# Optimization experiments

Hardware: AMD Instinct MI355X
Metric: run time of the kernel (lower is better)

The kernel has to match this reference:

```python
import jax, jax.numpy as jnp
import numpy as np

B, C, L, H, W = 4, 128, 8, 64, 64

def setup_inputs() -> dict:
    key = jax.random.key(0)
    ks = jax.random.split(key, 9)
    s = 0.05
    return {
        'feats': jax.random.normal(ks[0], (B, C, L, H, W), jnp.float32),
        'proj_w': jax.random.normal(ks[1], (C, C, L), jnp.float32) * s,  # Conv3d kernel (band,1,1) collapsing l
        'proj_b': jax.random.normal(ks[2], (C,), jnp.float32) * s,
        'w1': jax.random.normal(ks[3], (C, C), jnp.float32) * s,
        'b1': jax.random.normal(ks[4], (C,), jnp.float32) * s,
        'w2': jax.random.normal(ks[5], (C, C), jnp.float32) * s,
        'b2': jax.random.normal(ks[6], (C,), jnp.float32) * s,
        'w3': jax.random.normal(ks[7], (C, C), jnp.float32) * s,
        'b3': jax.random.normal(ks[8], (C,), jnp.float32) * s,
        'alpha': jnp.zeros((1,), jnp.float32),
    }

def reference(feats, proj_w, proj_b, w1, b1, w2, b2, w3, b3, alpha):
    b, c, l, h, w = feats.shape
    hw = h * w
    # CVT3D_2D_SA: 3D->2D projection, conv3d kernel (l,1,1) then squeeze
    f2d = jnp.einsum('bclhw,ocl->bohw', feats, proj_w) + proj_b[None, :, None, None]
    # 1x1 conv projections -> (b, c, hw)
    x = f2d.reshape(b, c, hw)
    q = jnp.einsum('bcn,oc->bon', x, w1) + b1[None, :, None]
    k = jnp.einsum('bcn,oc->bon', x, w2) + b2[None, :, None]
    v = jnp.einsum('bcn,oc->bon', x, w3) + b3[None, :, None]
    # scores[b,n,m] = sum_c q[b,c,n] * k[b,c,m]; softmax over m (dim=-1)
    scores = jnp.einsum('bcn,bcm->bnm', q, k)
    attn = jax.nn.softmax(scores, axis=-1)
    # feat_e[b,c,n] = sum_m v[b,c,m] * attn[b,n,m]
    feat_e = jnp.einsum('bcm,bnm->bcn', v, attn).reshape(b, c, h, w)
    # original computes out = alpha*feat_e + f2d but returns feat_e
    return feat_e
```

## Files before the change

### kernel.cpp

```cpp
#include <hip/hip_runtime.h>
#include <stdint.h>

typedef _Float16 h8 __attribute__((ext_vector_type(8)));
typedef _Float16 h4 __attribute__((ext_vector_type(4)));
typedef float f32x4 __attribute__((ext_vector_type(4)));
typedef float f32x16 __attribute__((ext_vector_type(16)));
typedef uint32_t u32x4 __attribute__((ext_vector_type(4)));

#if __has_builtin(__builtin_amdgcn_exp2f)
#define EXP2(x) __builtin_amdgcn_exp2f(x)
#else
#define EXP2(x) exp2f(x)
#endif

#if __has_builtin(__builtin_amdgcn_permlane32_swap)
#define HAVE_PLSWAP 1
#else
#define HAVE_PLSWAP 0
#endif

#define WS_PWH  0u
#define WS_WH   262144u
#define WS_BC   600064u
#define WS_F2D  1048576u
#define WS_OP   5242880u
#define WS_QKVT 38797312u
#define WS_VT   47185920u
#define WS_MLM  0u
#define WS_MLL  524288u

__device__ __forceinline__ void gll16(const void* g, void* l) {
  __builtin_amdgcn_global_load_lds((const __attribute__((address_space(1))) unsigned int*)g,
                                   (__attribute__((address_space(3))) unsigned int*)l, 16, 0, 0);
}

__global__ void k_cvt(const float* __restrict__ pw, const float* __restrict__ pb,
                      const float* __restrict__ w1, const float* __restrict__ b1,
                      const float* __restrict__ w2, const float* __restrict__ b2,
                      const float* __restrict__ w3, const float* __restrict__ b3,
                      _Float16* __restrict__ PWh, _Float16* __restrict__ Wh,
                      float* __restrict__ bc)
{
  const float LOG2E = 1.4426950408889634f;
  int idx = blockIdx.x * 256 + threadIdx.x;
  if (idx < 131072) {
    PWh[idx] = (_Float16)pw[idx];
  } else {
    int j = idx - 131072;
    if (j < 49152) {
      int g = j >> 14, rem = j & 16383;
      const float* wg = (g == 0) ? w1 : (g == 1 ? w2 : w3);
      float v = wg[rem];
      if (g == 0) v *= LOG2E;
      Wh[j] = (_Float16)v;
    }
  }
  if (idx < 384) {
    int g = idx >> 7, o = idx & 127;
    const float* wg = (g == 0) ? w1 : (g == 1 ? w2 : w3);
    const float* bg = (g == 0) ? b1 : (g == 1 ? b2 : b3);
    float s = bg[o];
    for (int c = 0; c < 128; ++c) s += wg[o * 128 + c] * pb[c];
    if (g == 0) s *= LOG2E;
    bc[idx] = s;
  }
}

#define FG1_LDS 51200
__global__ __launch_bounds__(256) void k_fg1(const float* __restrict__ feats,
                                             const _Float16* __restrict__ PWh,
                                             _Float16* __restrict__ f2d)
{
  extern __shared__ char smem[];
  const int t = threadIdx.x, lane = t & 63, w = t >> 6;
  const int lo = lane & 15, hi = lane >> 4;
  const int n0 = blockIdx.x * 32, b = blockIdx.y;
  const int wr = w >> 1, wc = w & 1;
  const char* pwc = (const char*)PWh;

  float4 areg[2];
  auto loadA = [&](int s) {
    #pragma unroll
    for (int p = 0; p < 2; ++p) {
      int i = t + p * 256, row = i >> 3, slot = i & 7;
      areg[p] = *(const float4*)(feats + ((size_t)(b * 1024 + s * 64 + row)) * 4096 + n0 + slot * 4);
    }
  };
  auto writeA = [&](int buf) {
    char* base = smem + buf * 9216;
    #pragma unroll
    for (int p = 0; p < 2; ++p) {
      int i = t + p * 256, row = i >> 3, slot = i & 7;
      *(float4*)(base + row * 144 + slot * 16) = areg[p];
    }
  };
  auto gllB = [&](int s, int buf) {
    char* base = smem + 18432 + buf * 16384;
    #pragma unroll
    for (int q = 0; q < 4; ++q) {
      int o = (w * 4 + q) * 8 + (lane >> 3);
      int slot = lane & 7;
      gll16(pwc + (size_t)o * 2048 + s * 128 + ((slot * 16) ^ ((o & 7) << 4)),
            base + (w * 4 + q) * 1024);
    }
  };

  const f32x4 zero4 = {0.f, 0.f, 0.f, 0.f};
  f32x4 acc[4];
  #pragma unroll
  for (int j2 = 0; j2 < 4; ++j2) acc[j2] = zero4;

  loadA(0); writeA(0); gllB(0, 0);
  for (int s = 0; s < 16; ++s) {
    __syncthreads();
    if (s < 15) { loadA(s + 1); gllB(s + 1, (s + 1) & 1); }
    const char* fb = smem + (s & 1) * 9216;
    const char* pb_ = smem + 18432 + (s & 1) * 16384;
    #pragma unroll
    for (int kk = 0; kk < 2; ++kk) {
      const int nl = wr * 16 + lo;
      float f0 = *(const float*)(fb + (kk * 32 + hi * 8 + 0) * 144 + nl * 4);
      float f1 = *(const float*)(fb + (kk * 32 + hi * 8 + 1) * 144 + nl * 4);
      float f2 = *(const float*)(fb + (kk * 32 + hi * 8 + 2) * 144 + nl * 4);
      float f3 = *(const float*)(fb + (kk * 32 + hi * 8 + 3) * 144 + nl * 4);
      float f4 = *(const float*)(fb + (kk * 32 + hi * 8 + 4) * 144 + nl * 4);
      float f5 = *(const float*)(fb + (kk * 32 + hi * 8 + 5) * 144 + nl * 4);
      float f6 = *(const float*)(fb + (kk * 32 + hi * 8 + 6) * 144 + nl * 4);
      float f7 = *(const float*)(fb + (kk * 32 + hi * 8 + 7) * 144 + nl * 4);
      u32x4 ua = { __builtin_bit_cast(uint32_t, __builtin_amdgcn_cvt_pkrtz(f0, f1)),
                   __builtin_bit_cast(uint32_t, __builtin_amdgcn_cvt_pkrtz(f2, f3)),
                   __builtin_bit_cast(uint32_t, __builtin_amdgcn_cvt_pkrtz(f4, f5)),
                   __builtin_bit_cast(uint32_t, __builtin_amdgcn_cvt_pkrtz(f6, f7)) };
      h8 af = __builtin_bit_cast(h8, ua);
      h8 bf[4];
      #pragma unroll
      for (int j2 = 0; j2 < 4; ++j2) {
        int o = wc * 64 + j2 * 16 + lo;
        bf[j2] = *(const h8*)(pb_ + o * 128 + ((kk * 64 + hi * 16) ^ ((o & 7) << 4)));
      }
      #pragma unroll
      for (int j2 = 0; j2 < 4; ++j2)
        acc[j2] = __builtin_amdgcn_mfma_f32_16x16x32_f16(af, bf[j2], acc[j2], 0, 0, 0);
    }
    if (s < 15) writeA((s + 1) & 1);
  }

  #pragma unroll
  for (int j2 = 0; j2 < 4; ++j2) {
    int o = wc * 64 + j2 * 16 + lo;
    #pragma unroll
    for (int r = 0; r < 4; ++r) {
      int n = n0 + wr * 16 + hi * 4 + r;
      f2d[((size_t)(b * 4096 + n)) * 128 + o] = (_Float16)acc[j2][r];
    }
  }
}

__global__ void k_gemm2(const _Float16* __restrict__ f2d, const _Float16* __restrict__ Wh,
                        const float* __restrict__ bc, _Float16* __restrict__ qkvt,
                        _Float16* __restrict__ vt)
{
  extern __shared__ char smem[];
  const int t = threadIdx.x, lane = t & 63, w = t >> 6;
  const int lo = lane & 15, hi = lane >> 4;
  const int bx = blockIdx.x, n0 = blockIdx.y * 128, b = blockIdx.z;
  const int wr = w >> 1, wc = w & 1;
  const int nb = wr * 64, ob = wc * 64;
  const char* f2c = (const char*)f2d;

  #pragma unroll
  for (int q = 0; q < 8; ++q) {
    int c = w * 8 + q;
    int row = c * 4 + (lane >> 4);
    int col = ((lane & 15) * 16) ^ ((row & 7) << 4);
    gll16(f2c + ((size_t)(b * 4096 + n0 + row)) * 256 + col, smem + c * 1024);
    gll16((const char*)Wh + (size_t)(bx * 128 + row) * 256 + col, smem + 32768 + c * 1024);
  }
  __syncthreads();

  const f32x4 zero4 = {0.f, 0.f, 0.f, 0.f};
  f32x4 acc[4][4];
  #pragma unroll
  for (int i2 = 0; i2 < 4; ++i2)
    #pragma unroll
    for (int j2 = 0; j2 < 4; ++j2) acc[i2][j2] = zero4;

  #pragma unroll
  for (int kk = 0; kk < 4; ++kk) {
    const int cb = kk * 64 + hi * 16;
    h8 af[4], bf[4];
    #pragma unroll
    for (int i2 = 0; i2 < 4; ++i2) {
      int row = nb + i2 * 16 + lo;
      af[i2] = *(const h8*)(smem + row * 256 + (cb ^ ((row & 7) << 4)));
    }
    #pragma unroll
    for (int j2 = 0; j2 < 4; ++j2) {
      int row = ob + j2 * 16 + lo;
      bf[j2] = *(const h8*)(smem + 32768 + row * 256 + (cb ^ ((row & 7) << 4)));
    }
    #pragma unroll
    for (int i2 = 0; i2 < 4; ++i2)
      #pragma unroll
      for (int j2 = 0; j2 < 4; ++j2)
        acc[i2][j2] = __builtin_amdgcn_mfma_f32_16x16x32_f16(af[i2], bf[j2], acc[i2][j2], 0, 0, 0);
  }

  if (bx < 2) {
    #pragma unroll
    for (int j2 = 0; j2 < 4; ++j2) {
      int o = bx * 128 + ob + j2 * 16 + lo;
      float bias = bc[o];
      #pragma unroll
      for (int i2 = 0; i2 < 4; ++i2)
        #pragma unroll
        for (int r = 0; r < 4; ++r) {
          int n = n0 + nb + i2 * 16 + hi * 4 + r;
          qkvt[((size_t)(b * 4096 + n)) * 256 + o] = (_Float16)(acc[i2][j2][r] + bias);
        }
    }
  } else {
    __syncthreads();
    #pragma unroll
    for (int j2 = 0; j2 < 4; ++j2) {
      int o = ob + j2 * 16 + lo;
      float bias = bc[256 + o];
      #pragma unroll
      for (int i2 = 0; i2 < 4; ++i2) {
        int nl = nb + i2 * 16 + hi * 4;
        h4 v4;
        #pragma unroll
        for (int r = 0; r < 4; ++r) v4[r] = (_Float16)(acc[i2][j2][r] + bias);
        *(h4*)(smem + o * 272 + nl * 2) = v4;
      }
    }
    __syncthreads();
    #pragma unroll
    for (int p2 = 0; p2 < 8; ++p2) {
      int i = t + p2 * 256, d = i >> 4, ch = i & 15;
      uint4 v = *(const uint4*)(smem + d * 272 + ch * 16);
      *(uint4*)((char*)vt + ((size_t)(b * 128 + d)) * 8192 + (n0 + ch * 8) * 2) = v;
    }
  }
}

#define ATT_LDS 32768
__global__ __launch_bounds__(256, 2) void k_attn_part(const _Float16* __restrict__ qkvt,
                                                      const _Float16* __restrict__ vt,
                                                      _Float16* __restrict__ opart,
                                                      float* __restrict__ mlm,
                                                      float* __restrict__ mll)
{
  extern __shared__ char smem[];
  const int t = threadIdx.x, lane = t & 63, w = t >> 6;
  const int q31 = lane & 31, h2 = lane >> 5;
  const int id = blockIdx.x;
  const int vid = (id & 7) * 64 + (id >> 3);
  const int qt = vid & 15, bp = vid >> 4;
  const int b = bp >> 3, p = bp & 7;
  const int n0 = qt * 256;
  const char* qbase = (const char*)qkvt + (size_t)b * 4096 * 512;
  const char* vbase = (const char*)vt + (size_t)b * 128 * 8192;

  h8 bq0[8], bq1[8];
  {
    const char* qr0 = qbase + (size_t)(n0 + w * 64 + q31) * 512;
    const char* qr1 = qbase + (size_t)(n0 + w * 64 + 32 + q31) * 512;
    #pragma unroll
    for (int dk = 0; dk < 8; ++dk) {
      bq0[dk] = *(const h8*)(qr0 + dk * 32 + h2 * 16);
      bq1[dk] = *(const h8*)(qr1 + dk * 32 + h2 * 16);
    }
  }

  int koff[2], voff[2], dst_[2];
  #pragma unroll
  for (int i = 0; i < 2; ++i) {
    int idx = t + i * 256;
    int krow = idx >> 4, ks = idx & 15;
    koff[i] = krow * 512 + 256 + ((ks ^ (krow & 7)) * 16);
    int vd = idx >> 2, vs = idx & 3;
    voff[i] = vd * 8192 + ((vs ^ ((vd >> 1) & 3)) * 16);
    dst_[i] = idx * 16;
  }

  auto stage = [&](int m0, int buf) {
    char* kb = smem + buf * 16384;
    char* vb = kb + 8192;
    #pragma unroll
    for (int i = 0; i < 2; ++i) {
      gll16(qbase + (size_t)m0 * 512 + koff[i], kb + dst_[i]);
      gll16(vbase + (size_t)m0 * 2 + voff[i], vb + dst_[i]);
    }
  };

  float m0r = -1e30f, l0r = 0.f, m1r = -1e30f, l1r = 0.f;
  f32x16 oacc0[4], oacc1[4];
  #pragma unroll
  for (int dt = 0; dt < 4; ++dt)
    #pragma unroll
    for (int r = 0; r < 16; ++r) { oacc0[dt][r] = 0.f; oacc1[dt][r] = 0.f; }

  const int base = p * 512;
  stage(base, 0);
  __syncthreads();

  for (int it = 0; it < 16; ++it) {
    const int buf = it & 1;
    if (it < 15) stage(base + (it + 1) * 32, buf ^ 1);

    const char* kb = smem + buf * 16384;
    const char* vb = kb + 8192;

    f32x16 s0, s1;
    #pragma unroll
    for (int r = 0; r < 16; ++r) { s0[r] = 0.f; s1[r] = 0.f; }
    __builtin_amdgcn_s_setprio(1);
    #pragma unroll
    for (int dk = 0; dk < 8; ++dk) {
      h8 ak = *(const h8*)(kb + q31 * 256 + (((dk * 2 + h2) ^ (q31 & 7)) * 16));
      s0 = __builtin_amdgcn_mfma_f32_32x32x16_f16(ak, bq0[dk], s0, 0, 0, 0);
      s1 = __builtin_amdgcn_mfma_f32_32x32x16_f16(ak, bq1[dk], s1, 0, 0, 0);
    }
    __builtin_amdgcn_s_setprio(0);

    h8 p0k0, p0k1, p1k0, p1k1;
    {
      float mxl = s0[0];
      #pragma unroll
      for (int r = 1; r < 16; ++r) mxl = fmaxf(mxl, s0[r]);
      if (__any(mxl > m0r + 8.f)) {
        float mq = fmaxf(mxl, __shfl_xor(mxl, 32));
        float mnew = fmaxf(m0r, mq);
        float scn = EXP2(m0r - mnew);
        m0r = mnew;
        l0r *= scn;
        #pragma unroll
        for (int dt = 0; dt < 4; ++dt)
          #pragma unroll
          for (int r = 0; r < 16; ++r) oacc0[dt][r] *= scn;
      }
      float pv[16], rs = 0.f;
      #pragma unroll
      for (int r = 0; r < 16; ++r) { pv[r] = EXP2(s0[r] - m0r); rs += pv[r]; }
      l0r += rs;
      uint32_t wd[8];
      #pragma unroll
      for (int j = 0; j < 8; ++j)
        wd[j] = __builtin_bit_cast(uint32_t, __builtin_amdgcn_cvt_pkrtz(pv[2 * j], pv[2 * j + 1]));
#if HAVE_PLSWAP
      auto r02 = __builtin_amdgcn_permlane32_swap(wd[0], wd[2], false, false);
      auto r13 = __builtin_amdgcn_permlane32_swap(wd[1], wd[3], false, false);
      auto r46 = __builtin_amdgcn_permlane32_swap(wd[4], wd[6], false, false);
      auto r57 = __builtin_amdgcn_permlane32_swap(wd[5], wd[7], false, false);
      u32x4 b0 = { r02[0], r13[0], r02[1], r13[1] };
      u32x4 b1 = { r46[0], r57[0], r46[1], r57[1] };
#else
      uint32_t xw[8];
      #pragma unroll
      for (int j = 0; j < 8; ++j) xw[j] = __shfl_xor(wd[j], 32);
      u32x4 b0 = { h2 ? xw[2] : wd[0], h2 ? xw[3] : wd[1],
                   h2 ? wd[2] : xw[0], h2 ? wd[3] : xw[1] };
      u32x4 b1 = { h2 ? xw[6] : wd[4], h2 ? xw[7] : wd[5],
                   h2 ? wd[6] : xw[4], h2 ? wd[7] : xw[5] };
#endif
      p0k0 = __builtin_bit_cast(h8, b0);
      p0k1 = __builtin_bit_cast(h8, b1);
    }
    {
      float mxl = s1[0];
      #pragma unroll
      for (int r = 1; r < 16; ++r) mxl = fmaxf(mxl, s1[r]);
      if (__any(mxl > m1r + 8.f)) {
        float mq = fmaxf(mxl, __shfl_xor(mxl, 32));
        float mnew = fmaxf(m1r, mq);
        float scn = EXP2(m1r - mnew);
        m1r = mnew;
        l1r *= scn;
        #pragma unroll
        for (int dt = 0; dt < 4; ++dt)
          #pragma unroll
          for (int r = 0; r < 16; ++r) oacc1[dt][r] *= scn;
      }
      float pv[16], rs = 0.f;
      #pragma unroll
      for (int r = 0; r < 16; ++r) { pv[r] = EXP2(s1[r] - m1r); rs += pv[r]; }
      l1r += rs;
      uint32_t wd[8];
      #pragma unroll
      for (int j = 0; j < 8; ++j)
        wd[j] = __builtin_bit_cast(uint32_t, __builtin_amdgcn_cvt_pkrtz(pv[2 * j], pv[2 * j + 1]));
#if HAVE_PLSWAP
      auto r02 = __builtin_amdgcn_permlane32_swap(wd[0], wd[2], false, false);
      auto r13 = __builtin_amdgcn_permlane32_swap(wd[1], wd[3], false, false);
      auto r46 = __builtin_amdgcn_permlane32_swap(wd[4], wd[6], false, false);
      auto r57 = __builtin_amdgcn_permlane32_swap(wd[5], wd[7], false, false);
      u32x4 b0 = { r02[0], r13[0], r02[1], r13[1] };
      u32x4 b1 = { r46[0], r57[0], r46[1], r57[1] };
#else
      uint32_t xw[8];
      #pragma unroll
      for (int j = 0; j < 8; ++j) xw[j] = __shfl_xor(wd[j], 32);
      u32x4 b0 = { h2 ? xw[2] : wd[0], h2 ? xw[3] : wd[1],
                   h2 ? wd[2] : xw[0], h2 ? wd[3] : xw[1] };
      u32x4 b1 = { h2 ? xw[6] : wd[4], h2 ? xw[7] : wd[5],
                   h2 ? wd[6] : xw[4], h2 ? wd[7] : xw[5] };
#endif
      p1k0 = __builtin_bit_cast(h8, b0);
      p1k1 = __builtin_bit_cast(h8, b1);
    }

    __builtin_amdgcn_s_setprio(1);
    #pragma unroll
    for (int ks = 0; ks < 2; ++ks) {
      #pragma unroll
      for (int dt = 0; dt < 4; ++dt) {
        int d = dt * 32 + q31;
        h8 av = *(const h8*)(vb + d * 64 + (((ks * 2 + h2) ^ ((d >> 1) & 3)) * 16));
        oacc0[dt] = __builtin_amdgcn_mfma_f32_32x32x16_f16(av, ks ? p0k1 : p0k0, oacc0[dt], 0, 0, 0);
        oacc1[dt] = __builtin_amdgcn_mfma_f32_32x32x16_f16(av, ks ? p1k1 : p1k0, oacc1[dt], 0, 0, 0);
      }
    }
    __builtin_amdgcn_s_setprio(0);

    if (it < 15) __syncthreads();
  }

  _Float16* oph = opart + ((size_t)(p * 4 + b) * 128) * 4096;
  l0r += __shfl_xor(l0r, 32);
  l1r += __shfl_xor(l1r, 32);
  float inv0 = 1.0f / l0r, inv1 = 1.0f / l1r;
  const int nc0 = n0 + w * 64 + q31, nc1 = nc0 + 32;
  #pragma unroll
  for (int dt = 0; dt < 4; ++dt)
    #pragma unroll
    for (int r = 0; r < 16; ++r) {
      int d = dt * 32 + (r & 3) + 8 * (r >> 2) + 4 * h2;
      oph[(size_t)d * 4096 + nc0] = (_Float16)(oacc0[dt][r] * inv0);
      oph[(size_t)d * 4096 + nc1] = (_Float16)(oacc1[dt][r] * inv1);
    }
  if (h2 == 0) {
    size_t mlb = (size_t)(p * 4 + b) * 4096;
    mlm[mlb + nc0] = m0r;  mll[mlb + nc0] = l0r;
    mlm[mlb + nc1] = m1r;  mll[mlb + nc1] = l1r;
  }
}

__global__ void k_reduce(const _Float16* __restrict__ opart, const float* __restrict__ mlm,
                         const float* __restrict__ mll, float* __restrict__ out)
{
  int idx = blockIdx.x * 256 + threadIdx.x;
  int n4 = idx & 1023, d = (idx >> 10) & 127, b = idx >> 17;
  int n0 = n4 * 4;
  f32x4 m[8], lv[8];
  #pragma unroll
  for (int p = 0; p < 8; ++p) {
    size_t mb = (size_t)(p * 4 + b) * 4096 + n0;
    m[p]  = *(const f32x4*)(mlm + mb);
    lv[p] = *(const f32x4*)(mll + mb);
  }
  f32x4 M = m[0];
  #pragma unroll
  for (int p = 1; p < 8; ++p)
    #pragma unroll
    for (int j = 0; j < 4; ++j) M[j] = fmaxf(M[j], m[p][j]);
  f32x4 denom = {0.f, 0.f, 0.f, 0.f}, num = {0.f, 0.f, 0.f, 0.f};
  #pragma unroll
  for (int p = 0; p < 8; ++p) {
    h4 o = *(const h4*)(opart + ((size_t)((p * 4 + b) * 128 + d)) * 4096 + n0);
    #pragma unroll
    for (int j = 0; j < 4; ++j) {
      float wgt = lv[p][j] * EXP2(m[p][j] - M[j]);
      denom[j] += wgt;
      num[j]   += (float)o[j] * wgt;
    }
  }
  f32x4 r;
  #pragma unroll
  for (int j = 0; j < 4; ++j) r[j] = num[j] / denom[j];
  *(f32x4*)(out + ((size_t)(b * 128 + d)) * 4096 + n0) = r;
}

extern "C" void kernel_launch(void* const* d_in, const int* in_sizes, int n_in,
                              void* d_out, int out_size, void* d_ws, size_t ws_size,
                              hipStream_t stream)
{
  const float* feats = (const float*)d_in[0];
  const float* pw = (const float*)d_in[1];
  const float* pb = (const float*)d_in[2];
  const float* w1 = (const float*)d_in[3];
  const float* b1 = (const float*)d_in[4];
  const float* w2 = (const float*)d_in[5];
  const float* b2 = (const float*)d_in[6];
  const float* w3 = (const float*)d_in[7];
  const float* b3 = (const float*)d_in[8];
  char* ws = (char*)d_ws;
  _Float16* PWh = (_Float16*)(ws + WS_PWH);
  _Float16* Wh = (_Float16*)(ws + WS_WH);
  float* bc = (float*)(ws + WS_BC);
  _Float16* f2d = (_Float16*)(ws + WS_F2D);
  _Float16* qkvt = (_Float16*)(ws + WS_QKVT);
  _Float16* vt = (_Float16*)(ws + WS_VT);
  _Float16* opart = (_Float16*)(ws + WS_OP);
  float* mlm = (float*)(ws + WS_MLM);
  float* mll = (float*)(ws + WS_MLL);
  float* out = (float*)d_out;

  hipLaunchKernelGGL(k_cvt, dim3(704), dim3(256), 0, stream,
                     pw, pb, w1, b1, w2, b2, w3, b3, PWh, Wh, bc);
  hipLaunchKernelGGL(k_fg1, dim3(128, 4), dim3(256), FG1_LDS, stream, feats, PWh, f2d);
  hipLaunchKernelGGL(k_gemm2, dim3(3, 32, 4), dim3(256), 65536, stream, f2d, Wh, bc, qkvt, vt);
  hipLaunchKernelGGL(k_attn_part, dim3(512), dim3(256), ATT_LDS, stream, qkvt, vt, opart, mlm, mll);
  hipLaunchKernelGGL(k_reduce, dim3(2048), dim3(256), 0, stream, opart, mlm, mll, out);
}
```

Before: 107.0 us.

## Parallelize bias fold, shrink projection tiles, widen gemm2 blocks, retune attention

The bias-fold loop in k_cvt moves from a serial 128-step loop in 384 threads onto extra wave-per-output blocks that use a shuffle reduction. k_fg1 halves its n-tile to 16 columns per block, doubling the block count and cutting LDS use. k_gemm2 runs 512 threads per block, so each wave computes half the rows. The attention kernel drops s_setprio, changes launch bounds to one block per SM, and uses a tree for the row max. Together these aim to shorten the serial bias computation and add parallelism to the small GEMMs, at the cost of less data reuse per block.

```diff
diff --git a/kernel.cpp b/kernel.cpp
--- a/kernel.cpp
+++ b/kernel.cpp
@@ -42,31 +42,39 @@
                       float* __restrict__ bc)
 {
   const float LOG2E = 1.4426950408889634f;
-  int idx = blockIdx.x * 256 + threadIdx.x;
-  if (idx < 131072) {
-    PWh[idx] = (_Float16)pw[idx];
+  const int blk = blockIdx.x;
+  if (blk < 704) {
+    int idx = blk * 256 + threadIdx.x;
+    if (idx < 131072) {
+      PWh[idx] = (_Float16)pw[idx];
+    } else {
+      int j = idx - 131072;
+      if (j < 49152) {
+        int g = j >> 14, rem = j & 16383;
+        const float* wg = (g == 0) ? w1 : (g == 1 ? w2 : w3);
+        float v = wg[rem];
+        if (g == 0) v *= LOG2E;
+        Wh[j] = (_Float16)v;
+      }
+    }
   } else {
-    int j = idx - 131072;
-    if (j < 49152) {
-      int g = j >> 14, rem = j & 16383;
-      const float* wg = (g == 0) ? w1 : (g == 1 ? w2 : w3);
-      float v = wg[rem];
-      if (g == 0) v *= LOG2E;
-      Wh[j] = (_Float16)v;
-    }
-  }
-  if (idx < 384) {
-    int g = idx >> 7, o = idx & 127;
+    int w = threadIdx.x >> 6, lane = threadIdx.x & 63;
+    int o3 = (blk - 704) * 4 + w;
+    int g = o3 >> 7, o = o3 & 127;
     const float* wg = (g == 0) ? w1 : (g == 1 ? w2 : w3);
     const float* bg = (g == 0) ? b1 : (g == 1 ? b2 : b3);
-    float s = bg[o];
-    for (int c = 0; c < 128; ++c) s += wg[o * 128 + c] * pb[c];
-    if (g == 0) s *= LOG2E;
-    bc[idx] = s;
-  }
-}
-
-#define FG1_LDS 51200
+    float s = wg[o * 128 + lane] * pb[lane] + wg[o * 128 + 64 + lane] * pb[64 + lane];
+    s += __shfl_xor(s, 1);  s += __shfl_xor(s, 2);  s += __shfl_xor(s, 4);
+    s += __shfl_xor(s, 8);  s += __shfl_xor(s, 16); s += __shfl_xor(s, 32);
+    if (lane == 0) {
+      float r = bg[o] + s;
+      if (g == 0) r *= LOG2E;
+      bc[o3] = r;
+    }
+  }
+}
+
+#define FG1_LDS 43008
 __global__ __launch_bounds__(256) void k_fg1(const float* __restrict__ feats,
                                              const _Float16* __restrict__ PWh,
                                              _Float16* __restrict__ f2d)
@@ -74,103 +82,95 @@
   extern __shared__ char smem[];
   const int t = threadIdx.x, lane = t & 63, w = t >> 6;
   const int lo = lane & 15, hi = lane >> 4;
-  const int n0 = blockIdx.x * 32, b = blockIdx.y;
-  const int wr = w >> 1, wc = w & 1;
+  const int n0 = blockIdx.x * 16, b = blockIdx.y;
   const char* pwc = (const char*)PWh;
 
-  float4 areg[2];
+  float4 areg;
+  const int arow = t >> 2, aslot = t & 3;
   auto loadA = [&](int s) {
-    #pragma unroll
-    for (int p = 0; p < 2; ++p) {
-      int i = t + p * 256, row = i >> 3, slot = i & 7;
-      areg[p] = *(const float4*)(feats + ((size_t)(b * 1024 + s * 64 + row)) * 4096 + n0 + slot * 4);
-    }
+    areg = *(const float4*)(feats + ((size_t)(b * 1024 + s * 64 + arow)) * 4096 + n0 + aslot * 4);
   };
   auto writeA = [&](int buf) {
-    char* base = smem + buf * 9216;
-    #pragma unroll
-    for (int p = 0; p < 2; ++p) {
-      int i = t + p * 256, row = i >> 3, slot = i & 7;
-      *(float4*)(base + row * 144 + slot * 16) = areg[p];
-    }
+    *(float4*)(smem + buf * 5120 + arow * 80 + aslot * 16) = areg;
   };
   auto gllB = [&](int s, int buf) {
-    char* base = smem + 18432 + buf * 16384;
+    char* base = smem + 10240 + buf * 16384;
     #pragma unroll
     for (int q = 0; q < 4; ++q) {
-      int o = (w * 4 + q) * 8 + (lane >> 3);
+      int c = w * 4 + q;
+      int o = c * 8 + (lane >> 3);
       int slot = lane & 7;
       gll16(pwc + (size_t)o * 2048 + s * 128 + ((slot * 16) ^ ((o & 7) << 4)),
-            base + (w * 4 + q) * 1024);
+            base + c * 1024);
     }
   };
 
   const f32x4 zero4 = {0.f, 0.f, 0.f, 0.f};
-  f32x4 acc[4];
-  #pragma unroll
-  for (int j2 = 0; j2 < 4; ++j2) acc[j2] = zero4;
+  f32x4 acc[2];
+  acc[0] = zero4; acc[1] = zero4;
 
   loadA(0); writeA(0); gllB(0, 0);
   for (int s = 0; s < 16; ++s) {
     __syncthreads();
     if (s < 15) { loadA(s + 1); gllB(s + 1, (s + 1) & 1); }
-    const char* fb = smem + (s & 1) * 9216;
-    const char* pb_ = smem + 18432 + (s & 1) * 16384;
+    const char* fb = smem + (s & 1) * 5120;
+    const char* pb_ = smem + 10240 + (s & 1) * 16384;
     #pragma unroll
     for (int kk = 0; kk < 2; ++kk) {
-      const int nl = wr * 16 + lo;
-      float f0 = *(const float*)(fb + (kk * 32 + hi * 8 + 0) * 144 + nl * 4);
-      float f1 = *(const float*)(fb + (kk * 32 + hi * 8 + 1) * 144 + nl * 4);
-      float f2 = *(const float*)(fb + (kk * 32 + hi * 8 + 2) * 144 + nl * 4);
-      float f3 = *(const float*)(fb + (kk * 32 + hi * 8 + 3) * 144 + nl * 4);
-      float f4 = *(const float*)(fb + (kk * 32 + hi * 8 + 4) * 144 + nl * 4);
-      float f5 = *(const float*)(fb + (kk * 32 + hi * 8 + 5) * 144 + nl * 4);
-      float f6 = *(const float*)(fb + (kk * 32 + hi * 8 + 6) * 144 + nl * 4);
-      float f7 = *(const float*)(fb + (kk * 32 + hi * 8 + 7) * 144 + nl * 4);
+      float f0 = *(const float*)(fb + (kk * 32 + hi * 8 + 0) * 80 + lo * 4);
+      float f1 = *(const float*)(fb + (kk * 32 + hi * 8 + 1) * 80 + lo * 4);
+      float f2 = *(const float*)(fb + (kk * 32 + hi * 8 + 2) * 80 + lo * 4);
+      float f3 = *(const float*)(fb + (kk * 32 + hi * 8 + 3) * 80 + lo * 4);
+      float f4 = *(const float*)(fb + (kk * 32 + hi * 8 + 4) * 80 + lo * 4);
+      float f5 = *(const float*)(fb + (kk * 32 + hi * 8 + 5) * 80 + lo * 4);
+      float f6 = *(const float*)(fb + (kk * 32 + hi * 8 + 6) * 80 + lo * 4);
+      float f7 = *(const float*)(fb + (kk * 32 + hi * 8 + 7) * 80 + lo * 4);
       u32x4 ua = { __builtin_bit_cast(uint32_t, __builtin_amdgcn_cvt_pkrtz(f0, f1)),
                    __builtin_bit_cast(uint32_t, __builtin_amdgcn_cvt_pkrtz(f2, f3)),
                    __builtin_bit_cast(uint32_t, __builtin_amdgcn_cvt_pkrtz(f4, f5)),
                    __builtin_bit_cast(uint32_t, __builtin_amdgcn_cvt_pkrtz(f6, f7)) };
       h8 af = __builtin_bit_cast(h8, ua);
-      h8 bf[4];
-      #pragma unroll
-      for (int j2 = 0; j2 < 4; ++j2) {
-        int o = wc * 64 + j2 * 16 + lo;
+      h8 bf[2];
+      #pragma unroll
+      for (int j2 = 0; j2 < 2; ++j2) {
+        int o = w * 32 + j2 * 16 + lo;
         bf[j2] = *(const h8*)(pb_ + o * 128 + ((kk * 64 + hi * 16) ^ ((o & 7) << 4)));
       }
       #pragma unroll
-      for (int j2 = 0; j2 < 4; ++j2)
+      for (int j2 = 0; j2 < 2; ++j2)
         acc[j2] = __builtin_amdgcn_mfma_f32_16x16x32_f16(af, bf[j2], acc[j2], 0, 0, 0);
     }
     if (s < 15) writeA((s + 1) & 1);
   }
 
   #pragma unroll
-  for (int j2 = 0; j2 < 4; ++j2) {
-    int o = wc * 64 + j2 * 16 + lo;
+  for (int j2 = 0; j2 < 2; ++j2) {
+    int o = w * 32 + j2 * 16 + lo;
     #pragma unroll
     for (int r = 0; r < 4; ++r) {
-      int n = n0 + wr * 16 + hi * 4 + r;
+      int n = n0 + hi * 4 + r;
       f2d[((size_t)(b * 4096 + n)) * 128 + o] = (_Float16)acc[j2][r];
     }
   }
 }
 
-__global__ void k_gemm2(const _Float16* __restrict__ f2d, const _Float16* __restrict__ Wh,
-                        const float* __restrict__ bc, _Float16* __restrict__ qkvt,
-                        _Float16* __restrict__ vt)
+__global__ __launch_bounds__(512) void k_gemm2(const _Float16* __restrict__ f2d,
+                                               const _Float16* __restrict__ Wh,
+                                               const float* __restrict__ bc,
+                                               _Float16* __restrict__ qkvt,
+                                               _Float16* __restrict__ vt)
 {
   extern __shared__ char smem[];
   const int t = threadIdx.x, lane = t & 63, w = t >> 6;
   const int lo = lane & 15, hi = lane >> 4;
   const int bx = blockIdx.x, n0 = blockIdx.y * 128, b = blockIdx.z;
   const int wr = w >> 1, wc = w & 1;
-  const int nb = wr * 64, ob = wc * 64;
+  const int nb = wr * 32, ob = wc * 64;
   const char* f2c = (const char*)f2d;
 
   #pragma unroll
-  for (int q = 0; q < 8; ++q) {
-    int c = w * 8 + q;
+  for (int q = 0; q < 4; ++q) {
+    int c = w * 4 + q;
     int row = c * 4 + (lane >> 4);
     int col = ((lane & 15) * 16) ^ ((row & 7) << 4);
     gll16(f2c + ((size_t)(b * 4096 + n0 + row)) * 256 + col, smem + c * 1024);
@@ -179,18 +179,18 @@
   __syncthreads();
 
   const f32x4 zero4 = {0.f, 0.f, 0.f, 0.f};
-  f32x4 acc[4][4];
-  #pragma unroll
-  for (int i2 = 0; i2 < 4; ++i2)
+  f32x4 acc[2][4];
+  #pragma unroll
+  for (int i2 = 0; i2 < 2; ++i2)
     #pragma unroll
     for (int j2 = 0; j2 < 4; ++j2) acc[i2][j2] = zero4;
 
   #pragma unroll
   for (int kk = 0; kk < 4; ++kk) {
     const int cb = kk * 64 + hi * 16;
-    h8 af[4], bf[4];
-    #pragma unroll
-    for (int i2 = 0; i2 < 4; ++i2) {
+    h8 af[2], bf[4];
+    #pragma unroll
+    for (int i2 = 0; i2 < 2; ++i2) {
       int row = nb + i2 * 16 + lo;
       af[i2] = *(const h8*)(smem + row * 256 + (cb ^ ((row & 7) << 4)));
     }
@@ -200,7 +200,7 @@
       bf[j2] = *(const h8*)(smem + 32768 + row * 256 + (cb ^ ((row & 7) << 4)));
     }
     #pragma unroll
-    for (int i2 = 0; i2 < 4; ++i2)
+    for (int i2 = 0; i2 < 2; ++i2)
       #pragma unroll
       for (int j2 = 0; j2 < 4; ++j2)
         acc[i2][j2] = __builtin_amdgcn_mfma_f32_16x16x32_f16(af[i2], bf[j2], acc[i2][j2], 0, 0, 0);
@@ -212,7 +212,7 @@
       int o = bx * 128 + ob + j2 * 16 + lo;
       float bias = bc[o];
       #pragma unroll
-      for (int i2 = 0; i2 < 4; ++i2)
+      for (int i2 = 0; i2 < 2; ++i2)
         #pragma unroll
         for (int r = 0; r < 4; ++r) {
           int n = n0 + nb + i2 * 16 + hi * 4 + r;
@@ -226,7 +226,7 @@
       int o = ob + j2 * 16 + lo;
       float bias = bc[256 + o];
       #pragma unroll
-      for (int i2 = 0; i2 < 4; ++i2) {
+      for (int i2 = 0; i2 < 2; ++i2) {
         int nl = nb + i2 * 16 + hi * 4;
         h4 v4;
         #pragma unroll
@@ -236,8 +236,8 @@
     }
     __syncthreads();
     #pragma unroll
-    for (int p2 = 0; p2 < 8; ++p2) {
-      int i = t + p2 * 256, d = i >> 4, ch = i & 15;
+    for (int p2 = 0; p2 < 4; ++p2) {
+      int i = t + p2 * 512, d = i >> 4, ch = i & 15;
       uint4 v = *(const uint4*)(smem + d * 272 + ch * 16);
       *(uint4*)((char*)vt + ((size_t)(b * 128 + d)) * 8192 + (n0 + ch * 8) * 2) = v;
     }
@@ -245,7 +245,7 @@
 }
 
 #define ATT_LDS 32768
-__global__ __launch_bounds__(256, 2) void k_attn_part(const _Float16* __restrict__ qkvt,
+__global__ __launch_bounds__(256, 1) void k_attn_part(const _Float16* __restrict__ qkvt,
                                                       const _Float16* __restrict__ vt,
                                                       _Float16* __restrict__ opart,
                                                       float* __restrict__ mlm,
@@ -315,20 +315,21 @@
     f32x16 s0, s1;
     #pragma unroll
     for (int r = 0; r < 16; ++r) { s0[r] = 0.f; s1[r] = 0.f; }
-    __builtin_amdgcn_s_setprio(1);
     #pragma unroll
     for (int dk = 0; dk < 8; ++dk) {
       h8 ak = *(const h8*)(kb + q31 * 256 + (((dk * 2 + h2) ^ (q31 & 7)) * 16));
       s0 = __builtin_amdgcn_mfma_f32_32x32x16_f16(ak, bq0[dk], s0, 0, 0, 0);
       s1 = __builtin_amdgcn_mfma_f32_32x32x16_f16(ak, bq1[dk], s1, 0, 0, 0);
     }
-    __builtin_amdgcn_s_setprio(0);
 
     h8 p0k0, p0k1, p1k0, p1k1;
     {
-      float mxl = s0[0];
-      #pragma unroll
-      for (int r = 1; r < 16; ++r) mxl = fmaxf(mxl, s0[r]);
+      float t0 = fmaxf(fmaxf(s0[0],  s0[1]),  s0[2]);
+      float t1 = fmaxf(fmaxf(s0[3],  s0[4]),  s0[5]);
+      float t2 = fmaxf(fmaxf(s0[6],  s0[7]),  s0[8]);
+      float t3 = fmaxf(fmaxf(s0[9],  s0[10]), s0[11]);
+      float t4 = fmaxf(fmaxf(s0[12], s0[13]), s0[14]);
+      float mxl = fmaxf(fmaxf(fmaxf(t0, t1), t2), fmaxf(fmaxf(t3, t4), s0[15]));
       if (__any(mxl > m0r + 8.f)) {
         float mq = fmaxf(mxl, __shfl_xor(mxl, 32));
         float mnew = fmaxf(m0r, mq);
@@ -368,9 +369,12 @@
       p0k1 = __builtin_bit_cast(h8, b1);
     }
     {
-      float mxl = s1[0];
-      #pragma unroll
-      for (int r = 1; r < 16; ++r) mxl = fmaxf(mxl, s1[r]);
+      float t0 = fmaxf(fmaxf(s1[0],  s1[1]),  s1[2]);
+      float t1 = fmaxf(fmaxf(s1[3],  s1[4]),  s1[5]);
+      float t2 = fmaxf(fmaxf(s1[6],  s1[7]),  s1[8]);
+      float t3 = fmaxf(fmaxf(s1[9],  s1[10]), s1[11]);
+      float t4 = fmaxf(fmaxf(s1[12], s1[13]), s1[14]);
+      float mxl = fmaxf(fmaxf(fmaxf(t0, t1), t2), fmaxf(fmaxf(t3, t4), s1[15]));
       if (__any(mxl > m1r + 8.f)) {
         float mq = fmaxf(mxl, __shfl_xor(mxl, 32));
         float mnew = fmaxf(m1r, mq);
@@ -410,7 +414,6 @@
       p1k1 = __builtin_bit_cast(h8, b1);
     }
 
-    __builtin_amdgcn_s_setprio(1);
     #pragma unroll
     for (int ks = 0; ks < 2; ++ks) {
       #pragma unroll
@@ -421,7 +424,6 @@
         oacc1[dt] = __builtin_amdgcn_mfma_f32_32x32x16_f16(av, ks ? p1k1 : p1k0, oacc1[dt], 0, 0, 0);
       }
     }
-    __builtin_amdgcn_s_setprio(0);
 
     if (it < 15) __syncthreads();
   }
@@ -506,10 +508,10 @@
   float* mll = (float*)(ws + WS_MLL);
   float* out = (float*)d_out;
 
-  hipLaunchKernelGGL(k_cvt, dim3(704), dim3(256), 0, stream,
+  hipLaunchKernelGGL(k_cvt, dim3(800), dim3(256), 0, stream,
                      pw, pb, w1, b1, w2, b2, w3, b3, PWh, Wh, bc);
-  hipLaunchKernelGGL(k_fg1, dim3(128, 4), dim3(256), FG1_LDS, stream, feats, PWh, f2d);
-  hipLaunchKernelGGL(k_gemm2, dim3(3, 32, 4), dim3(256), 65536, stream, f2d, Wh, bc, qkvt, vt);
+  hipLaunchKernelGGL(k_fg1, dim3(256, 4), dim3(256), FG1_LDS, stream, feats, PWh, f2d);
+  hipLaunchKernelGGL(k_gemm2, dim3(3, 32, 4), dim3(512), 65536, stream, f2d, Wh, bc, qkvt, vt);
   hipLaunchKernelGGL(k_attn_part, dim3(512), dim3(256), ATT_LDS, stream, qkvt, vt, opart, mlm, mll);
   hipLaunchKernelGGL(k_reduce, dim3(2048), dim3(256), 0, stream, opart, mlm, mll, out);
 }
```

New measurement: 121.0 us. 1.13x slower.
